# Kernel tuning notes

Hardware: AMD Instinct MI355X
Metric: run time of the kernel (lower is better)

## Reference

```python
import jax, jax.numpy as jnp
import numpy as np

B, S, D, H, DH, BS, L, R, V, FF = 4, 4096, 768, 12, 64, 64, 2, 3, 50257, 3072
NB = S // BS          # 64 key/query blocks
NSEL = 5 + R          # 2 global + 3 window + R random key blocks per query block


def layer_norm(x, g, b, eps=1e-12):
    m = jnp.mean(x, axis=-1, keepdims=True)
    v = jnp.mean(jnp.square(x - m), axis=-1, keepdims=True)
    return (x - m) * jax.lax.rsqrt(v + eps) * g + b


def setup_inputs() -> dict:
    key = jax.random.key(0)
    ks = iter(jax.random.split(key, 16))
    p = lambda shape: jax.random.normal(next(ks), shape, jnp.float32) * 0.02
    return {
        'input_ids': jax.random.randint(next(ks), (B, S), 0, V, jnp.int32),
        'attention_mask': jnp.ones((B, S), jnp.int32),
        'label': jax.random.randint(next(ks), (B,), 0, 2, jnp.int32),
        'rand_idx': jax.random.randint(next(ks), (NB, R), 0, NB, jnp.int32),
        'emb': p((V, D)), 'pos_emb': p((S, D)),
        'ln_emb_g': jnp.ones((D,)), 'ln_emb_b': jnp.zeros((D,)),
        'Wqkv': p((L, D, 3 * D)), 'bqkv': jnp.zeros((L, 3 * D)),
        'Wo': p((L, D, D)), 'bo': jnp.zeros((L, D)),
        'ln1_g': jnp.ones((L, D)), 'ln1_b': jnp.zeros((L, D)),
        'Wff1': p((L, D, FF)), 'bff1': jnp.zeros((L, FF)),
        'Wff2': p((L, FF, D)), 'bff2': jnp.zeros((L, D)),
        'ln2_g': jnp.ones((L, D)), 'ln2_b': jnp.zeros((L, D)),
        'Wp': p((D, D)), 'bp': jnp.zeros((D,)),
        'Wc': p((D, 2)), 'bc': jnp.zeros((2,)),
    }


def reference(input_ids, attention_mask, label, rand_idx, emb, pos_emb,
              ln_emb_g, ln_emb_b, Wqkv, bqkv, Wo, bo, ln1_g, ln1_b,
              Wff1, bff1, Wff2, bff2, ln2_g, ln2_b, Wp, bp, Wc, bc):
    blk = jnp.arange(NB, dtype=jnp.int32)
    sel = jnp.concatenate([
        jnp.zeros((NB, 1), jnp.int32),
        ((blk - 1) % NB)[:, None], blk[:, None], ((blk + 1) % NB)[:, None],
        jnp.full((NB, 1), NB - 1, jnp.int32),
        rand_idx.astype(jnp.int32),
    ], axis=1)  # [NB, NSEL]

    h = emb[input_ids] + pos_emb[None]                 # [B,S,D]
    h = layer_norm(h, ln_emb_g, ln_emb_b)

    mblk = attention_mask.reshape(B, NB, BS)
    mask_sel = mblk[:, sel].reshape(B, 1, NB, 1, NSEL * BS)  # gathered key mask
    bias = jnp.where(mask_sel > 0, 0.0, -1e9).astype(h.dtype)

    scale = 1.0 / np.sqrt(DH)
    for l in range(L):
        qkv = h @ Wqkv[l] + bqkv[l]
        q, k, v = jnp.split(qkv, 3, axis=-1)
        to_blocks = lambda t: t.reshape(B, NB, BS, H, DH).transpose(0, 3, 1, 2, 4)  # [B,H,NB,BS,DH]
        qb, kb, vb = to_blocks(q), to_blocks(k), to_blocks(v)
        ksel = kb[:, :, sel].reshape(B, H, NB, NSEL * BS, DH)  # gather sparse key blocks
        vsel = vb[:, :, sel].reshape(B, H, NB, NSEL * BS, DH)
        scores = jnp.einsum('bhnqd,bhnkd->bhnqk', qb, ksel) * scale + bias
        attn = jax.nn.softmax(scores, axis=-1)
        ob = jnp.einsum('bhnqk,bhnkd->bhnqd', attn, vsel)
        o = ob.transpose(0, 2, 3, 1, 4).reshape(B, S, D)
        h = layer_norm(h + o @ Wo[l] + bo[l], ln1_g[l], ln1_b[l])
        ff = jax.nn.gelu(h @ Wff1[l] + bff1[l]) @ Wff2[l] + bff2[l]
        h = layer_norm(h + ff, ln2_g[l], ln2_b[l])

    pooled = jnp.tanh(h[:, 0] @ Wp + bp)               # BERT-style pooler on [CLS]
    probs = jax.nn.softmax(pooled @ Wc + bc, axis=1)
    # Faithful to the original: CrossEntropyLoss applied to softmax OUTPUT (double softmax)
    loss = -jnp.mean(jax.nn.log_softmax(probs, axis=1)[jnp.arange(B), label])
    return probs, loss
```

## Files before the change

kernel.cpp:

```cpp
#include <hip/hip_runtime.h>
#include <hip/hip_bf16.h>
#include <stdint.h>


using bf16 = __hip_bfloat16;
typedef __bf16 bf16x8 __attribute__((ext_vector_type(8)));
typedef __bf16 bf16x4 __attribute__((ext_vector_type(4)));
typedef float f32x4 __attribute__((ext_vector_type(4)));

__device__ __forceinline__ float b2f(bf16 x) { return __bfloat162float(x); }
__device__ __forceinline__ bf16 f2b(float x) { return __float2bfloat16(x); }
__device__ __forceinline__ float ldf(const void* p, size_t i, int flag) {
  return flag ? __bfloat162float(((const bf16*)p)[i]) : ((const float*)p)[i];
}

__device__ __forceinline__ void gld_lds16(const bf16* g, bf16* l) {
  __builtin_amdgcn_global_load_lds((__attribute__((address_space(1))) void*)g,
                                   (__attribute__((address_space(3))) void*)l, 16, 0, 0);
}

__device__ __forceinline__ f32x4 mfma16(bf16x8 a, bf16x8 b, f32x4 c) {
  return __builtin_amdgcn_mfma_f32_16x16x32_bf16(a, b, c, 0, 0, 0);
}

__device__ __forceinline__ float gelu_f(float x) {
  const float z = 1.5957691216057308f * (x + 0.044715f * x * x * x);
  return x / (1.0f + __expf(-z));
}

__global__ void probe_kernel(const uint32_t* __restrict__ g, int* __restrict__ flag) {
  if (threadIdx.x == 0) flag[0] = (g[0] == 0x3F803F80u) ? 1 : 0;
}

__global__ __launch_bounds__(256) void transpose_k(const void* __restrict__ in, size_t in_off,
                                                   bf16* __restrict__ out, int K, int N,
                                                   const int* __restrict__ dflag) {
  __shared__ float tile[32][33];
  const int flag = dflag[0];
  const int bx = blockIdx.x * 32;
  const int by = blockIdx.y * 32;
  const int tx = threadIdx.x & 31, ty = threadIdx.x >> 5;
#pragma unroll
  for (int i = 0; i < 32; i += 8)
    tile[ty + i][tx] = ldf(in, in_off + (size_t)(by + ty + i) * N + bx + tx, flag);
  __syncthreads();
#pragma unroll
  for (int i = 0; i < 32; i += 8)
    out[(size_t)(bx + ty + i) * K + by + tx] = f2b(tile[tx][ty + i]);
}

__global__ __launch_bounds__(256) void embed_ln_kernel(
    const int* __restrict__ ids, const void* __restrict__ emb, const void* __restrict__ pos,
    const void* __restrict__ g, const void* __restrict__ bb, bf16* __restrict__ h,
    const int* __restrict__ dflag) {
  __shared__ float red[8];
  const int flag = dflag[0];
  const int tok = blockIdx.x;
  const int tid = threadIdx.x;
  const int s = tok & 4095;
  const size_t id = (size_t)ids[tok];
  float v[3]; float sum = 0.f, sq = 0.f;
#pragma unroll
  for (int i = 0; i < 3; i++) {
    const int d = tid + i * 256;
    v[i] = ldf(emb, id * 768 + d, flag) + ldf(pos, (size_t)s * 768 + d, flag);
    sum += v[i]; sq += v[i] * v[i];
  }
#pragma unroll
  for (int off = 32; off >= 1; off >>= 1) { sum += __shfl_down(sum, off); sq += __shfl_down(sq, off); }
  if ((tid & 63) == 0) { red[(tid >> 6) * 2] = sum; red[(tid >> 6) * 2 + 1] = sq; }
  __syncthreads();
  sum = red[0] + red[2] + red[4] + red[6];
  sq  = red[1] + red[3] + red[5] + red[7];
  const float mean = sum * (1.0f / 768.0f);
  const float var = sq * (1.0f / 768.0f) - mean * mean;
  const float rs = rsqrtf(var + 1e-12f);
  bf16* hr = h + (size_t)tok * 768;
#pragma unroll
  for (int i = 0; i < 3; i++) {
    const int d = tid + i * 256;
    hr[d] = f2b((v[i] - mean) * rs * ldf(g, d, flag) + ldf(bb, d, flag));
  }
}

__global__ __launch_bounds__(256) void add_ln_kernel(
    bf16* __restrict__ h, const bf16* __restrict__ x,
    const void* __restrict__ g, const void* __restrict__ bb, size_t goff,
    const int* __restrict__ dflag) {
  __shared__ float red[8];
  const int flag = dflag[0];
  const int tok = blockIdx.x;
  const int tid = threadIdx.x;
  const size_t base = (size_t)tok * 768;
  float v[3]; float sum = 0.f, sq = 0.f;
#pragma unroll
  for (int i = 0; i < 3; i++) {
    const int d = tid + i * 256;
    v[i] = b2f(h[base + d]) + b2f(x[base + d]);
    sum += v[i]; sq += v[i] * v[i];
  }
#pragma unroll
  for (int off = 32; off >= 1; off >>= 1) { sum += __shfl_down(sum, off); sq += __shfl_down(sq, off); }
  if ((tid & 63) == 0) { red[(tid >> 6) * 2] = sum; red[(tid >> 6) * 2 + 1] = sq; }
  __syncthreads();
  sum = red[0] + red[2] + red[4] + red[6];
  sq  = red[1] + red[3] + red[5] + red[7];
  const float mean = sum * (1.0f / 768.0f);
  const float var = sq * (1.0f / 768.0f) - mean * mean;
  const float rs = rsqrtf(var + 1e-12f);
#pragma unroll
  for (int i = 0; i < 3; i++) {
    const int d = tid + i * 256;
    h[base + d] = f2b((v[i] - mean) * rs * ldf(g, goff + d, flag) + ldf(bb, goff + d, flag));
  }
}

template <int EPI, bool ABLK>
__global__ __launch_bounds__(256) void gemm_bt(
    const bf16* __restrict__ A, const bf16* __restrict__ Bt,
    const void* __restrict__ bias, size_t bias_off, bf16* __restrict__ C,
    int N, int K,
    bf16* __restrict__ qout, bf16* __restrict__ kout, bf16* __restrict__ vout,
    const int* __restrict__ dflag) {
  __shared__ __align__(16) bf16 smem[9216];
  bf16* sA = smem;
  bf16* sB = smem + 4096;
  const int m0 = blockIdx.x * 128;
  const int n0 = blockIdx.y * 128;
  const int tid = threadIdx.x;
  const int lane = tid & 63;
  const int wv = tid >> 6;
  const int wm = wv >> 1, wn = wv & 1;
  const int col = lane & 15, quad = lane >> 4;

  f32x4 acc[4][4] = {};

  const int sr = tid >> 2;
  const int kc = ((tid & 3) - ((tid >> 4) & 3)) & 3;
  const int sc = kc * 8;
  const bf16* gA = A + (size_t)(m0 + sr) * K + sc;
  const bf16* gB = Bt + (size_t)(n0 + sr) * K + sc;
  const size_t rstep = (size_t)64 * K;

  size_t cb0 = 0, cb1 = 0;
  if constexpr (ABLK) {
    const int t0 = m0 + sr, t1 = t0 + 64;
    cb0 = (size_t)(t0 >> 12) * 3145728 + ((t0 >> 6) & 63) * 4096 + (t0 & 63) * 64;
    cb1 = (size_t)(t1 >> 12) * 3145728 + ((t1 >> 6) & 63) * 4096 + (t1 & 63) * 64;
  }

  const int sl = (quad + (col >> 2)) & 3;

  for (int k0 = 0; k0 < K; k0 += 32) {
    const bf16 *pA0, *pA1;
    if constexpr (ABLK) {
      const int c = k0 + sc;
      const int hh = c >> 6, dh = c & 63;
      pA0 = A + cb0 + hh * 262144 + dh;
      pA1 = A + cb1 + hh * 262144 + dh;
    } else {
      pA0 = gA; pA1 = gA + rstep; gA += 32;
    }
    gld_lds16(pA0, sA + tid * 8);
    gld_lds16(pA1, sA + 2048 + tid * 8);
    gld_lds16(gB, sB + tid * 8);
    gld_lds16(gB + rstep, sB + 2048 + tid * 8);
    gB += 32;
    __syncthreads();
    bf16x8 av[4], bv[4];
#pragma unroll
    for (int t = 0; t < 4; t++)
      av[t] = *(const bf16x8*)(sA + (wm * 64 + t * 16 + col) * 32 + sl * 8);
#pragma unroll
    for (int t = 0; t < 4; t++)
      bv[t] = *(const bf16x8*)(sB + (wn * 64 + t * 16 + col) * 32 + sl * 8);
#pragma unroll
    for (int mt = 0; mt < 4; mt++)
#pragma unroll
      for (int nt = 0; nt < 4; nt++)
        acc[mt][nt] = mfma16(av[mt], bv[nt], acc[mt][nt]);
    __syncthreads();
  }

  const int flag = dflag[0];
  float bsv[4];
#pragma unroll
  for (int nt = 0; nt < 4; nt++)
    bsv[nt] = ldf(bias, bias_off + n0 + wn * 64 + nt * 16 + col, flag);

  if constexpr (EPI != 2) {
    for (int half = 0; half < 2; half++) {
      __syncthreads();
      if (wm == half) {
#pragma unroll
        for (int nt = 0; nt < 4; nt++)
#pragma unroll
          for (int mt = 0; mt < 4; mt++)
#pragma unroll
            for (int r = 0; r < 4; r++) {
              float val = acc[mt][nt][r] + bsv[nt];
              if constexpr (EPI == 1) val = gelu_f(val);
              smem[(mt * 16 + quad * 4 + r) * 136 + wn * 64 + nt * 16 + col] = f2b(val);
            }
      }
      __syncthreads();
#pragma unroll
      for (int rr = 0; rr < 4; rr++) {
        const int row = rr * 16 + (tid >> 4);
        const int ch = tid & 15;
        const bf16x8 vv = *(const bf16x8*)(smem + row * 136 + ch * 8);
        *(bf16x8*)(C + (size_t)(m0 + half * 64 + row) * N + n0 + ch * 8) = vv;
      }
    }
  } else {
    const int part = (n0 >= 1536) ? 2 : ((n0 >= 768) ? 1 : 0);
    const int w0 = n0 - part * 768;
    const int h0 = w0 >> 6;
    const int bb = m0 >> 12;
    for (int half = 0; half < 2; half++) {
      const int nb_ = ((m0 >> 6) & 63) + half;
      __syncthreads();
      if (wm == half) {
        if (part < 2) {
#pragma unroll
          for (int nt = 0; nt < 4; nt++)
#pragma unroll
            for (int mt = 0; mt < 4; mt++)
#pragma unroll
              for (int r = 0; r < 4; r++)
                smem[(mt * 16 + quad * 4 + r) * 136 + wn * 64 + nt * 16 + col] =
                    f2b(acc[mt][nt][r] + bsv[nt]);
        } else {
#pragma unroll
          for (int nt = 0; nt < 4; nt++) {
            const int ncol = wn * 64 + nt * 16 + col;
#pragma unroll
            for (int mt = 0; mt < 4; mt++) {
              bf16x4 pk;
#pragma unroll
              for (int r = 0; r < 4; r++) pk[r] = f2b(acc[mt][nt][r] + bsv[nt]);
              *(bf16x4*)(smem + ncol * 72 + mt * 16 + quad * 4) = pk;
            }
          }
        }
      }
      __syncthreads();
      const int j = tid >> 7;
      const size_t dbase = (size_t)((bb * 12 + h0 + j) * 64 + nb_) * 4096;
      if (part < 2) {
        bf16* dst = (part == 0) ? qout : kout;
#pragma unroll
        for (int rr = 0; rr < 4; rr++) {
          const int tsk = (tid & 127) + rr * 128;
          const int row = tsk >> 3, pc = tsk & 7;
          const bf16x8 vv = *(const bf16x8*)(smem + row * 136 + j * 64 + pc * 8);
          *(bf16x8*)(dst + dbase + row * 64 + pc * 8) = vv;
        }
      } else {
#pragma unroll
        for (int rr = 0; rr < 4; rr++) {
          const int tsk = (tid & 127) + rr * 128;
          const int dh = tsk >> 3, pc = tsk & 7;
          const bf16x8 vv = *(const bf16x8*)(smem + (j * 64 + dh) * 72 + pc * 8);
          *(bf16x8*)(vout + dbase + dh * 64 + pc * 8) = vv;
        }
      }
    }
  }
}

__global__ __launch_bounds__(256) void attn_kernel(
    const bf16* q, const bf16* __restrict__ kmat, const bf16* __restrict__ vT,
    const int* __restrict__ amask, const int* __restrict__ rand_idx, bf16* o) {
  __shared__ __align__(16) bf16 plds[4][16][32];
  const int idx = blockIdx.x;
  const int nb = idx & 63;
  const int bh = idx >> 6;
  const int bb = bh / 12;
  const int tid = threadIdx.x;
  const int wv = tid >> 6, lane = tid & 63;
  const int col = lane & 15, quad = lane >> 4;

  int sel[8];
  sel[0] = 0; sel[1] = (nb + 63) & 63; sel[2] = nb; sel[3] = (nb + 1) & 63;
  sel[4] = 63;
  sel[5] = rand_idx[nb * 3 + 0];
  sel[6] = rand_idx[nb * 3 + 1];
  sel[7] = rand_idx[nb * 3 + 2];

  const size_t bhbase = (size_t)bh * 64;
  const bf16* qb = q + (bhbase + nb) * 4096;
  const int qrow = wv * 16 + col;
  const bf16x8 aq0 = *(const bf16x8*)(qb + qrow * 64 + quad * 8);
  const bf16x8 aq1 = *(const bf16x8*)(qb + qrow * 64 + 32 + quad * 8);

  float sreg[32][4];
#pragma unroll
  for (int sb = 0; sb < 8; sb++) {
    const bf16* kb = kmat + (bhbase + sel[sb]) * 4096;
    const int* mrow = amask + bb * 4096 + sel[sb] * 64;
#pragma unroll
    for (int c = 0; c < 4; c++) {
      const int kr = c * 16 + col;
      const bf16x8 bk0 = *(const bf16x8*)(kb + kr * 64 + quad * 8);
      const bf16x8 bk1 = *(const bf16x8*)(kb + kr * 64 + 32 + quad * 8);
      f32x4 t = {};
      t = mfma16(aq0, bk0, t);
      t = mfma16(aq1, bk1, t);
      const float bias = (mrow[kr] > 0) ? 0.0f : -1e9f;
      const int ti = sb * 4 + c;
#pragma unroll
      for (int r = 0; r < 4; r++) sreg[ti][r] = t[r] * 0.125f + bias;
    }
  }

  float mx[4] = {-1e30f, -1e30f, -1e30f, -1e30f};
#pragma unroll
  for (int ti = 0; ti < 32; ti++)
#pragma unroll
    for (int r = 0; r < 4; r++) mx[r] = fmaxf(mx[r], sreg[ti][r]);
#pragma unroll
  for (int off = 8; off >= 1; off >>= 1)
#pragma unroll
    for (int r = 0; r < 4; r++) mx[r] = fmaxf(mx[r], __shfl_xor(mx[r], off));

  float sm[4] = {0.f, 0.f, 0.f, 0.f};
#pragma unroll
  for (int ti = 0; ti < 32; ti++)
#pragma unroll
    for (int r = 0; r < 4; r++) {
      const float p = __expf(sreg[ti][r] - mx[r]);
      sreg[ti][r] = p; sm[r] += p;
    }
#pragma unroll
  for (int off = 8; off >= 1; off >>= 1)
#pragma unroll
    for (int r = 0; r < 4; r++) sm[r] += __shfl_xor(sm[r], off);
  float inv[4];
#pragma unroll
  for (int r = 0; r < 4; r++) inv[r] = 1.0f / sm[r];

  f32x4 oacc[4] = {};
#pragma unroll
  for (int kc = 0; kc < 16; kc++) {
    __syncthreads();
#pragma unroll
    for (int j = 0; j < 2; j++)
#pragma unroll
      for (int r = 0; r < 4; r++)
        plds[wv][quad * 4 + r][j * 16 + col] = f2b(sreg[kc * 2 + j][r] * inv[r]);
    __syncthreads();
    const bf16x8 ap = *(const bf16x8*)(&plds[wv][col][quad * 8]);
    const int sb = kc >> 1;
    const int koff = (kc & 1) * 32 + quad * 8;
    const bf16* vb = vT + (bhbase + sel[sb]) * 4096;
#pragma unroll
    for (int nt = 0; nt < 4; nt++) {
      const bf16x8 bvv = *(const bf16x8*)(vb + (nt * 16 + col) * 64 + koff);
      oacc[nt] = mfma16(ap, bvv, oacc[nt]);
    }
  }

  bf16* ob = o + (bhbase + nb) * 4096;
#pragma unroll
  for (int nt = 0; nt < 4; nt++)
#pragma unroll
    for (int r = 0; r < 4; r++)
      ob[(wv * 16 + quad * 4 + r) * 64 + nt * 16 + col] = f2b(oacc[nt][r]);
}

__global__ __launch_bounds__(768) void pooler_kernel(
    const bf16* __restrict__ h, const void* __restrict__ Wp,
    const void* __restrict__ bp, float* __restrict__ pooled,
    const int* __restrict__ dflag) {
  __shared__ float hrow[768];
  const int flag = dflag[0];
  const int bb = blockIdx.x;
  const int j = threadIdx.x;
  hrow[j] = b2f(h[(size_t)bb * 4096 * 768 + j]);
  __syncthreads();
  float acc = 0.0f;
#pragma unroll 8
  for (int d = 0; d < 768; d++) acc += hrow[d] * ldf(Wp, (size_t)d * 768 + j, flag);
  pooled[bb * 768 + j] = tanhf(acc + ldf(bp, j, flag));
}

__global__ __launch_bounds__(256) void cls_kernel(
    const float* __restrict__ pooled, const void* __restrict__ Wc, const void* __restrict__ bc,
    const int* __restrict__ label, void* __restrict__ out, const int* __restrict__ dflag) {
  __shared__ float lsum[8];
  const int flag = dflag[0];
  const int tid = threadIdx.x;
  const int p = tid >> 5, i = tid & 31;
  const int bb = p >> 1, c = p & 1;
  float acc = 0.0f;
  for (int d = i; d < 768; d += 32) acc += pooled[bb * 768 + d] * ldf(Wc, (size_t)d * 2 + c, flag);
#pragma unroll
  for (int off = 16; off >= 1; off >>= 1) acc += __shfl_xor(acc, off);
  if (i == 0) lsum[p] = acc;
  __syncthreads();
  if (tid == 0) {
    float res[9];
    float loss = 0.0f;
    for (int b = 0; b < 4; b++) {
      const float l0 = lsum[b * 2 + 0] + ldf(bc, 0, flag);
      const float l1 = lsum[b * 2 + 1] + ldf(bc, 1, flag);
      const float m = fmaxf(l0, l1);
      const float e0 = expf(l0 - m), e1 = expf(l1 - m);
      const float s = e0 + e1;
      const float p0 = e0 / s, p1 = e1 / s;
      res[b * 2] = p0; res[b * 2 + 1] = p1;
      const float mm = fmaxf(p0, p1);
      const float lse = mm + logf(expf(p0 - mm) + expf(p1 - mm));
      const float chosen = (label[b] == 0) ? p0 : p1;
      loss -= (chosen - lse);
    }
    res[8] = loss * 0.25f;
    if (flag) { bf16* o = (bf16*)out; for (int j = 0; j < 9; j++) o[j] = f2b(res[j]); }
    else      { float* o = (float*)out; for (int j = 0; j < 9; j++) o[j] = res[j]; }
  }
}

extern "C" void kernel_launch(void* const* d_in, const int* in_sizes, int n_in,
                              void* d_out, int out_size, void* d_ws, size_t ws_size,
                              hipStream_t stream) {
  const int* input_ids      = (const int*)d_in[0];
  const int* attention_mask = (const int*)d_in[1];
  const int* label          = (const int*)d_in[2];
  const int* rand_idx       = (const int*)d_in[3];
  const void* emb      = d_in[4];
  const void* pos_emb  = d_in[5];
  const void* ln_emb_g = d_in[6];
  const void* ln_emb_b = d_in[7];
  const void* Wqkv = d_in[8];
  const void* bqkv = d_in[9];
  const void* Wo   = d_in[10];
  const void* bo   = d_in[11];
  const void* ln1_g = d_in[12];
  const void* ln1_b = d_in[13];
  const void* Wff1 = d_in[14];
  const void* bff1 = d_in[15];
  const void* Wff2 = d_in[16];
  const void* bff2 = d_in[17];
  const void* ln2_g = d_in[18];
  const void* ln2_b = d_in[19];
  const void* Wp = d_in[20];
  const void* bp = d_in[21];
  const void* Wc = d_in[22];
  const void* bc = d_in[23];

  bf16* ws = (bf16*)d_ws;
  size_t off = 0;
  int* dflag = (int*)(ws + off); off += 8;
  bf16* WqkvT = ws + off; off += (size_t)2 * 2304 * 768;
  bf16* WoT   = ws + off; off += (size_t)2 * 768 * 768;
  bf16* Wff1T = ws + off; off += (size_t)2 * 3072 * 768;
  bf16* Wff2T = ws + off; off += (size_t)2 * 768 * 3072;
  bf16* hbuf  = ws + off; off += (size_t)16384 * 768;
  bf16* qo    = ws + off; off += (size_t)16384 * 768;
  bf16* kbf   = ws + off; off += (size_t)16384 * 768;
  bf16* vbf   = ws + off; off += (size_t)16384 * 768;
  bf16* xbf   = ws + off; off += (size_t)16384 * 768;
  bf16* a1buf = ws + off; off += (size_t)16384 * 3072;
  float* pooled = (float*)(ws + off); off += 6144;

  dim3 blk(256);

  probe_kernel<<<1, 64, 0, stream>>>((const uint32_t*)ln_emb_g, dflag);

  for (int l = 0; l < 2; l++) {
    transpose_k<<<dim3(72, 24), blk, 0, stream>>>(Wqkv, (size_t)l * 768 * 2304, WqkvT + (size_t)l * 2304 * 768, 768, 2304, dflag);
    transpose_k<<<dim3(24, 24), blk, 0, stream>>>(Wo, (size_t)l * 768 * 768, WoT + (size_t)l * 768 * 768, 768, 768, dflag);
    transpose_k<<<dim3(96, 24), blk, 0, stream>>>(Wff1, (size_t)l * 768 * 3072, Wff1T + (size_t)l * 3072 * 768, 768, 3072, dflag);
    transpose_k<<<dim3(24, 96), blk, 0, stream>>>(Wff2, (size_t)l * 3072 * 768, Wff2T + (size_t)l * 768 * 3072, 3072, 768, dflag);
  }

  embed_ln_kernel<<<16384, blk, 0, stream>>>(input_ids, emb, pos_emb, ln_emb_g, ln_emb_b, hbuf, dflag);

  for (int l = 0; l < 2; l++) {
    gemm_bt<2, false><<<dim3(128, 18), blk, 0, stream>>>(hbuf, WqkvT + (size_t)l * 2304 * 768, bqkv, (size_t)l * 2304,
                                                         nullptr, 2304, 768, qo, kbf, vbf, dflag);
    attn_kernel<<<3072, blk, 0, stream>>>(qo, kbf, vbf, attention_mask, rand_idx, qo);
    gemm_bt<0, true><<<dim3(128, 6), blk, 0, stream>>>(qo, WoT + (size_t)l * 768 * 768, bo, (size_t)l * 768,
                                                       xbf, 768, 768, nullptr, nullptr, nullptr, dflag);
    add_ln_kernel<<<16384, blk, 0, stream>>>(hbuf, xbf, ln1_g, ln1_b, (size_t)l * 768, dflag);
    gemm_bt<1, false><<<dim3(128, 24), blk, 0, stream>>>(hbuf, Wff1T + (size_t)l * 3072 * 768, bff1, (size_t)l * 3072,
                                                         a1buf, 3072, 768, nullptr, nullptr, nullptr, dflag);
    gemm_bt<0, false><<<dim3(128, 6), blk, 0, stream>>>(a1buf, Wff2T + (size_t)l * 768 * 3072, bff2, (size_t)l * 768,
                                                        xbf, 768, 3072, nullptr, nullptr, nullptr, dflag);
    add_ln_kernel<<<16384, blk, 0, stream>>>(hbuf, xbf, ln2_g, ln2_b, (size_t)l * 768, dflag);
  }

  pooler_kernel<<<4, dim3(768), 0, stream>>>(hbuf, Wp, bp, pooled, dflag);
  cls_kernel<<<1, blk, 0, stream>>>(pooled, Wc, bc, label, d_out, dflag);

  (void)in_sizes; (void)n_in; (void)out_size; (void)ws_size;
}
```

Measured before the change: 1.793 ms.

## Rewrite sparse attention as online-softmax with double-buffered LDS K/V staging

The attention kernel now stages each selected K and V block into swizzled LDS buffers with async global-to-LDS loads, double-buffered so the next block loads while the current one computes. Softmax becomes an online (running max/sum) formulation per key block, computing S^T so probabilities land directly in MFMA operand registers and the per-chunk LDS round trip with two barriers is gone. The mask is precomputed as ballots so fully unmasked blocks skip the bias work. It adds LDS use (32KB) and manual vmcnt waits, which could limit occupancy or be fragile.

Result: faster. 1.545 ms (-13.8%).

```diff
diff --git a/kernel.cpp b/kernel.cpp
--- a/kernel.cpp
+++ b/kernel.cpp
@@ -10,6 +10,10 @@
 
 __device__ __forceinline__ float b2f(bf16 x) { return __bfloat162float(x); }
 __device__ __forceinline__ bf16 f2b(float x) { return __float2bfloat16(x); }
+__device__ __forceinline__ __bf16 f2br(float x) {
+  bf16 h = __float2bfloat16(x);
+  return *reinterpret_cast<__bf16*>(&h);
+}
 __device__ __forceinline__ float ldf(const void* p, size_t i, int flag) {
   return flag ? __bfloat162float(((const bf16*)p)[i]) : ((const float*)p)[i];
 }
@@ -238,7 +242,7 @@
             for (int mt = 0; mt < 4; mt++) {
               bf16x4 pk;
 #pragma unroll
-              for (int r = 0; r < 4; r++) pk[r] = f2b(acc[mt][nt][r] + bsv[nt]);
+              for (int r = 0; r < 4; r++) pk[r] = f2br(acc[mt][nt][r] + bsv[nt]);
               *(bf16x4*)(smem + ncol * 72 + mt * 16 + quad * 4) = pk;
             }
           }
@@ -269,10 +273,11 @@
   }
 }
 
-__global__ __launch_bounds__(256) void attn_kernel(
+__global__ __launch_bounds__(256, 4) void attn_kernel(
     const bf16* q, const bf16* __restrict__ kmat, const bf16* __restrict__ vT,
     const int* __restrict__ amask, const int* __restrict__ rand_idx, bf16* o) {
-  __shared__ __align__(16) bf16 plds[4][16][32];
+  __shared__ __align__(16) bf16 sK[2][4096];
+  __shared__ __align__(16) bf16 sV[2][4096];
   const int idx = blockIdx.x;
   const int nb = idx & 63;
   const int bh = idx >> 6;
@@ -289,84 +294,134 @@
   sel[7] = rand_idx[nb * 3 + 2];
 
   const size_t bhbase = (size_t)bh * 64;
+
   const bf16* qb = q + (bhbase + nb) * 4096;
   const int qrow = wv * 16 + col;
-  const bf16x8 aq0 = *(const bf16x8*)(qb + qrow * 64 + quad * 8);
-  const bf16x8 aq1 = *(const bf16x8*)(qb + qrow * 64 + 32 + quad * 8);
-
-  float sreg[32][4];
+  const bf16x8 bq0 = *(const bf16x8*)(qb + qrow * 64 + quad * 8);
+  const bf16x8 bq1 = *(const bf16x8*)(qb + qrow * 64 + 32 + quad * 8);
+
+  unsigned long long bal[8];
+#pragma unroll
+  for (int sb = 0; sb < 8; sb++)
+    bal[sb] = __ballot(amask[bb * 4096 + sel[sb] * 64 + lane] > 0);
+
+  const int srow = tid >> 3, sslot = tid & 7;
+  const int sw0 = ((sslot ^ (srow & 7)) << 3);
+
+  auto stage = [&](int buf, int blk) {
+    const bf16* gk = kmat + (bhbase + blk) * 4096;
+    const bf16* gv = vT + (bhbase + blk) * 4096;
+    bf16* dk = sK[buf];
+    bf16* dv = sV[buf];
+    gld_lds16(gk + srow * 64 + sw0, dk + tid * 8);
+    gld_lds16(gk + (srow + 32) * 64 + sw0, dk + 2048 + tid * 8);
+    gld_lds16(gv + srow * 64 + sw0, dv + tid * 8);
+    gld_lds16(gv + (srow + 32) * 64 + sw0, dv + 2048 + tid * 8);
+  };
+
+  f32x4 oacc[4] = {};
+  float mrun = -1e30f, lrun = 0.0f;
+
+  stage(0, sel[0]);
+
 #pragma unroll
   for (int sb = 0; sb < 8; sb++) {
-    const bf16* kb = kmat + (bhbase + sel[sb]) * 4096;
-    const int* mrow = amask + bb * 4096 + sel[sb] * 64;
+    const int cur = sb & 1;
+    if (sb < 7) {
+      stage(cur ^ 1, sel[sb + 1]);
+      asm volatile("s_waitcnt vmcnt(4)" ::: "memory");
+    } else {
+      asm volatile("s_waitcnt vmcnt(0)" ::: "memory");
+    }
+    __builtin_amdgcn_s_barrier();
+    asm volatile("" ::: "memory");
+
+    const bf16* kb = sK[cur];
+    f32x4 t[4];
 #pragma unroll
     for (int c = 0; c < 4; c++) {
-      const int kr = c * 16 + col;
-      const bf16x8 bk0 = *(const bf16x8*)(kb + kr * 64 + quad * 8);
-      const bf16x8 bk1 = *(const bf16x8*)(kb + kr * 64 + 32 + quad * 8);
-      f32x4 t = {};
-      t = mfma16(aq0, bk0, t);
-      t = mfma16(aq1, bk1, t);
-      const float bias = (mrow[kr] > 0) ? 0.0f : -1e9f;
-      const int ti = sb * 4 + c;
-#pragma unroll
-      for (int r = 0; r < 4; r++) sreg[ti][r] = t[r] * 0.125f + bias;
-    }
-  }
-
-  float mx[4] = {-1e30f, -1e30f, -1e30f, -1e30f};
-#pragma unroll
-  for (int ti = 0; ti < 32; ti++)
-#pragma unroll
-    for (int r = 0; r < 4; r++) mx[r] = fmaxf(mx[r], sreg[ti][r]);
-#pragma unroll
-  for (int off = 8; off >= 1; off >>= 1)
-#pragma unroll
-    for (int r = 0; r < 4; r++) mx[r] = fmaxf(mx[r], __shfl_xor(mx[r], off));
-
-  float sm[4] = {0.f, 0.f, 0.f, 0.f};
-#pragma unroll
-  for (int ti = 0; ti < 32; ti++)
-#pragma unroll
-    for (int r = 0; r < 4; r++) {
-      const float p = __expf(sreg[ti][r] - mx[r]);
-      sreg[ti][r] = p; sm[r] += p;
-    }
-#pragma unroll
-  for (int off = 8; off >= 1; off >>= 1)
-#pragma unroll
-    for (int r = 0; r < 4; r++) sm[r] += __shfl_xor(sm[r], off);
-  float inv[4];
-#pragma unroll
-  for (int r = 0; r < 4; r++) inv[r] = 1.0f / sm[r];
-
-  f32x4 oacc[4] = {};
-#pragma unroll
-  for (int kc = 0; kc < 16; kc++) {
-    __syncthreads();
-#pragma unroll
-    for (int j = 0; j < 2; j++)
-#pragma unroll
-      for (int r = 0; r < 4; r++)
-        plds[wv][quad * 4 + r][j * 16 + col] = f2b(sreg[kc * 2 + j][r] * inv[r]);
-    __syncthreads();
-    const bf16x8 ap = *(const bf16x8*)(&plds[wv][col][quad * 8]);
-    const int sb = kc >> 1;
-    const int koff = (kc & 1) * 32 + quad * 8;
-    const bf16* vb = vT + (bhbase + sel[sb]) * 4096;
-#pragma unroll
-    for (int nt = 0; nt < 4; nt++) {
-      const bf16x8 bvv = *(const bf16x8*)(vb + (nt * 16 + col) * 64 + koff);
-      oacc[nt] = mfma16(ap, bvv, oacc[nt]);
-    }
-  }
-
+      const int r = c * 16 + col;
+      const bf16x8 ak0 = *(const bf16x8*)(kb + r * 64 + ((quad ^ (r & 7)) << 3));
+      const bf16x8 ak1 = *(const bf16x8*)(kb + r * 64 + (((4 + quad) ^ (r & 7)) << 3));
+      f32x4 s4 = {};
+      s4 = mfma16(ak0, bq0, s4);
+      s4 = mfma16(ak1, bq1, s4);
+      t[c] = s4;
+    }
+#pragma unroll
+    for (int c = 0; c < 4; c++)
+#pragma unroll
+      for (int r = 0; r < 4; r++) t[c][r] *= 0.125f;
+    if (bal[sb] != ~0ull) {
+#pragma unroll
+      for (int c = 0; c < 4; c++)
+#pragma unroll
+        for (int r = 0; r < 4; r++)
+          if (!((bal[sb] >> (c * 16 + quad * 4 + r)) & 1)) t[c][r] -= 1e9f;
+    }
+
+    float pm = t[0][0];
+#pragma unroll
+    for (int c = 0; c < 4; c++)
+#pragma unroll
+      for (int r = 0; r < 4; r++) pm = fmaxf(pm, t[c][r]);
+    pm = fmaxf(pm, __shfl_xor(pm, 16));
+    pm = fmaxf(pm, __shfl_xor(pm, 32));
+
+    const float mnew = fmaxf(mrun, pm);
+    const float scale = __expf(mrun - mnew);
+    float ps = 0.0f;
+    bf16x8 pa8[2];
+#pragma unroll
+    for (int c = 0; c < 4; c++)
+#pragma unroll
+      for (int r = 0; r < 4; r++) {
+        const float p = __expf(t[c][r] - mnew);
+        ps += p;
+        pa8[c >> 1][(c & 1) * 4 + r] = f2br(p);
+      }
+    ps += __shfl_xor(ps, 16);
+    ps += __shfl_xor(ps, 32);
+    lrun = lrun * scale + ps;
+    mrun = mnew;
+
+    float sc[4];
+#pragma unroll
+    for (int r = 0; r < 4; r++) sc[r] = __shfl(scale, quad * 4 + r);
+#pragma unroll
+    for (int nt = 0; nt < 4; nt++)
+#pragma unroll
+      for (int r = 0; r < 4; r++) oacc[nt][r] *= sc[r];
+
+    const bf16* vb = sV[cur];
+#pragma unroll
+    for (int pr = 0; pr < 2; pr++) {
+      const int g0 = 4 * pr + (quad >> 1);
+      const int g1 = g0 + 2;
+      const int so = (quad & 1) * 4;
+#pragma unroll
+      for (int nt = 0; nt < 4; nt++) {
+        const int dh = nt * 16 + col;
+        const bf16x4 bv0 = *(const bf16x4*)(vb + dh * 64 + ((g0 ^ (col & 7)) << 3) + so);
+        const bf16x4 bv1 = *(const bf16x4*)(vb + dh * 64 + ((g1 ^ (col & 7)) << 3) + so);
+        const bf16x8 bv8 = __builtin_shufflevector(bv0, bv1, 0, 1, 2, 3, 4, 5, 6, 7);
+        oacc[nt] = mfma16(pa8[pr], bv8, oacc[nt]);
+      }
+    }
+    asm volatile("" ::: "memory");
+    __builtin_amdgcn_s_barrier();
+  }
+
+  const float invl = 1.0f / lrun;
+  float iv[4];
+#pragma unroll
+  for (int r = 0; r < 4; r++) iv[r] = __shfl(invl, quad * 4 + r);
   bf16* ob = o + (bhbase + nb) * 4096;
 #pragma unroll
   for (int nt = 0; nt < 4; nt++)
 #pragma unroll
     for (int r = 0; r < 4; r++)
-      ob[(wv * 16 + quad * 4 + r) * 64 + nt * 16 + col] = f2b(oacc[nt][r]);
+      ob[(wv * 16 + quad * 4 + r) * 64 + nt * 16 + col] = f2b(oacc[nt][r] * iv[r]);
 }
 
 __global__ __launch_bounds__(768) void pooler_kernel(
```
